# Performance work log

Measured on AMD Instinct MI355X. Metric: run time of the kernel, lower is better.

## Reference

```python
import jax, jax.numpy as jnp
import numpy as np

NUM_SLOTS = 24
EPS = 1e-5

def setup_inputs() -> dict:
    key = jax.random.key(0)
    k1, k2 = jax.random.split(key)
    x = jax.random.normal(k1, (4, 32, 200, 2048), dtype=jnp.float32)
    time = jax.random.randint(k2, (4, 2048), 0, NUM_SLOTS, dtype=jnp.int64)
    return {"x": x, "time": time}

def reference(x, time):
    # x: [b, c, n, t]; time: [b, t] int slot ids in [0, NUM_SLOTS)
    b, c, n, t = x.shape
    time = time[..., -t:]
    idx = time.reshape(b * t)

    # [b*t, n, c] layout matching x.permute(2,0,3,1).reshape(n, b*t, c) contraction
    xf = jnp.transpose(x, (0, 3, 2, 1)).reshape(b * t, n * c)

    # True segment-sum replaces the one-hot matmul; column L1-normalize == divide by slot count
    counts = jax.ops.segment_sum(jnp.ones((b * t,), x.dtype), idx, num_segments=NUM_SLOTS)
    denom = jnp.maximum(counts, 1e-12)[:, None]  # F.normalize eps-clamped norm

    sum_x = jax.ops.segment_sum(xf, idx, num_segments=NUM_SLOTS)            # [S, n*c]
    sum_x2 = jax.ops.segment_sum(xf * xf, idx, num_segments=NUM_SLOTS)      # [S, n*c]

    mean_slot = (sum_x / denom).reshape(NUM_SLOTS, n, c).mean(axis=1)       # [S, c]
    m2_slot = (sum_x2 / denom).reshape(NUM_SLOTS, n, c).mean(axis=1)        # [S, c]
    var_slot = m2_slot - mean_slot ** 2                                     # [S, c]

    # Embedding gather back per (b, t), broadcast over n
    sm = jnp.transpose(mean_slot[time], (0, 2, 1))[:, :, None, :]           # [b, c, 1, t]
    sv = jnp.transpose(var_slot[time], (0, 2, 1))[:, :, None, :]            # [b, c, 1, t]

    return (x - sm) / jnp.sqrt(sv + EPS)
```

## Files before the change

### kernel.cpp

```cpp
#include <hip/hip_runtime.h>
#include <math.h>

#define Bb 4
#define Cc 32
#define Nn 200
#define Tt 2048
#define Ss 24
#define EPSf 1e-5f

typedef float f4 __attribute__((ext_vector_type(4)));
typedef int i4 __attribute__((ext_vector_type(4)));


__global__ __launch_bounds__(1024) void k_prep(const int* __restrict__ timei,
                                               float* __restrict__ gss,
                                               int* __restrict__ hist) {
    __shared__ int lh[Ss];
    const int tid = threadIdx.x;
    if (tid < Ss) lh[tid] = 0;
    for (int i = tid; i < 2 * Ss * Cc; i += 1024) gss[i] = 0.0f;
    __syncthreads();
    for (int i = tid; i < Bb * Tt; i += 1024) atomicAdd(&lh[timei[i]], 1);
    __syncthreads();
    if (tid < Ss) hist[tid] = lh[tid];
}

__global__ __launch_bounds__(256) void k_partial(const float* __restrict__ x,
                                                 const int* __restrict__ timei,
                                                 float* __restrict__ gsum,
                                                 float* __restrict__ gsq) {
    __shared__ float lsum[Ss];
    __shared__ float lsq[Ss];
    const int tid = threadIdx.x;
    const int bx  = blockIdx.x;
    const int tt = bx & 1;
    const int nc = (bx >> 1) & 7;
    const int bc = bx >> 4;
    const int b  = bc >> 5;
    const int c  = bc & 31;

    if (tid < Ss) { lsum[tid] = 0.0f; lsq[tid] = 0.0f; }
    __syncthreads();

    const int t0 = tt * 1024 + tid * 4;
    const i4 sl = *(const i4*)(timei + b * Tt + t0);

    const float* base = x + ((size_t)((b * Cc + c) * Nn)) * Tt + t0;
    float s0 = 0.f, s1 = 0.f, s2 = 0.f, s3 = 0.f;
    float q0 = 0.f, q1 = 0.f, q2 = 0.f, q3 = 0.f;
    const int n0 = nc * 25;
#pragma unroll 5
    for (int n = n0; n < n0 + 25; ++n) {
        f4 v = *(const f4*)(base + (size_t)n * Tt);
        s0 += v[0]; q0 += v[0] * v[0];
        s1 += v[1]; q1 += v[1] * v[1];
        s2 += v[2]; q2 += v[2] * v[2];
        s3 += v[3]; q3 += v[3] * v[3];
    }
    atomicAdd(&lsum[sl[0]], s0); atomicAdd(&lsq[sl[0]], q0);
    atomicAdd(&lsum[sl[1]], s1); atomicAdd(&lsq[sl[1]], q1);
    atomicAdd(&lsum[sl[2]], s2); atomicAdd(&lsq[sl[2]], q2);
    atomicAdd(&lsum[sl[3]], s3); atomicAdd(&lsq[sl[3]], q3);
    __syncthreads();

    if (tid < Ss) {
        atomicAdd(&gsum[tid * Cc + c], lsum[tid]);
        atomicAdd(&gsq[tid * Cc + c], lsq[tid]);
    }
}

__global__ __launch_bounds__(256) void k_norm(const float* __restrict__ x,
                                              const int* __restrict__ timei,
                                              const float* __restrict__ gsum,
                                              const float* __restrict__ gsq,
                                              const int* __restrict__ hist,
                                              float* __restrict__ out) {
    __shared__ float sm[Ss];
    __shared__ float sr[Ss];
    __shared__ float mt[Tt];
    __shared__ float rt[Tt];
    const int tid = threadIdx.x;
    const int idx = (Bb * Cc * 25 - 1) - blockIdx.x;
    const int nchunk = idx % 25;
    const int c = (idx / 25) & 31;
    const int b = idx / (25 * 32);

    if (tid < Ss) {
        float cnt   = (float)hist[tid];
        float denom = fmaxf(cnt, 1e-12f) * (float)Nn;
        float m     = gsum[tid * Cc + c] / denom;
        float m2    = gsq[tid * Cc + c] / denom;
        sm[tid] = m;
        sr[tid] = 1.0f / sqrtf(m2 - m * m + EPSf);
    }
    __syncthreads();

    for (int t = tid; t < Tt; t += 256) {
        const int s = timei[b * Tt + t];
        mt[t] = sm[s];
        rt[t] = sr[s];
    }
    __syncthreads();

    const size_t plane = (size_t)(b * Cc + c) * Nn;
    const int nbeg = nchunk * 8;
#pragma unroll
    for (int n = nbeg; n < nbeg + 8; ++n) {
        const float* xr = x + (plane + n) * Tt;
        float* orow = out + (plane + n) * Tt;
        for (int t4 = tid * 4; t4 < Tt; t4 += 1024) {
            f4 v = *(const f4*)(xr + t4);
            f4 m = *(const f4*)(&mt[t4]);
            f4 r = *(const f4*)(&rt[t4]);
            f4 o;
            o[0] = (v[0] - m[0]) * r[0];
            o[1] = (v[1] - m[1]) * r[1];
            o[2] = (v[2] - m[2]) * r[2];
            o[3] = (v[3] - m[3]) * r[3];
            __builtin_nontemporal_store(o, (f4*)(orow + t4));
        }
    }
}

extern "C" void kernel_launch(void* const* d_in, const int* in_sizes, int n_in,
                              void* d_out, int out_size, void* d_ws, size_t ws_size,
                              hipStream_t stream) {
    const float* x   = (const float*)d_in[0];
    const int* timei = (const int*)d_in[1];
    float* out  = (float*)d_out;
    float* ws   = (float*)d_ws;
    float* gsum = ws;
    float* gsq  = ws + Ss * Cc;
    int*   hist = (int*)(ws + 2 * Ss * Cc);

    k_prep<<<1, 1024, 0, stream>>>(timei, ws, hist);
    k_partial<<<2048, 256, 0, stream>>>(x, timei, gsum, gsq);
    k_norm<<<Bb * Cc * 25, 256, 0, stream>>>(x, timei, gsum, gsq, hist, out);
}
```

Measured before the change: 120.3 us.

## Drop prep kernel, write per-chunk partials, reduce stats inside normalize blocks

Removes the single-block prep kernel by folding the slot histogram into a subset of stats blocks and replacing global float atomics with per-chunk partial writes. The normalize kernel now reduces those partials itself and computes per-slot scale and shift. It also keeps per-thread slot coefficients in registers rather than staging per-t tables in shared memory, and uses an FMA form. Normalize blocks are much larger (50 rows each, 512 blocks), which cuts redundant partial reductions but lowers parallelism and tail flexibility.

```diff
diff --git a/kernel.cpp b/kernel.cpp
--- a/kernel.cpp
+++ b/kernel.cpp
@@ -12,25 +12,12 @@
 typedef int i4 __attribute__((ext_vector_type(4)));
 
 
-__global__ __launch_bounds__(1024) void k_prep(const int* __restrict__ timei,
-                                               float* __restrict__ gss,
-                                               int* __restrict__ hist) {
-    __shared__ int lh[Ss];
-    const int tid = threadIdx.x;
-    if (tid < Ss) lh[tid] = 0;
-    for (int i = tid; i < 2 * Ss * Cc; i += 1024) gss[i] = 0.0f;
-    __syncthreads();
-    for (int i = tid; i < Bb * Tt; i += 1024) atomicAdd(&lh[timei[i]], 1);
-    __syncthreads();
-    if (tid < Ss) hist[tid] = lh[tid];
-}
-
-__global__ __launch_bounds__(256) void k_partial(const float* __restrict__ x,
-                                                 const int* __restrict__ timei,
-                                                 float* __restrict__ gsum,
-                                                 float* __restrict__ gsq) {
-    __shared__ float lsum[Ss];
-    __shared__ float lsq[Ss];
+__global__ __launch_bounds__(256) void k_stats(const float* __restrict__ x,
+                                               const int* __restrict__ timei,
+                                               float2* __restrict__ part,
+                                               int* __restrict__ cntpart) {
+    __shared__ float lsum[Ss], lsq[Ss];
+    __shared__ int   lcnt[Ss];
     const int tid = threadIdx.x;
     const int bx  = blockIdx.x;
     const int tt = bx & 1;
@@ -38,87 +25,114 @@
     const int bc = bx >> 4;
     const int b  = bc >> 5;
     const int c  = bc & 31;
+    const bool do_hist = (c == 0 && nc == 0);
 
-    if (tid < Ss) { lsum[tid] = 0.0f; lsq[tid] = 0.0f; }
+    if (tid < Ss) { lsum[tid] = 0.f; lsq[tid] = 0.f; lcnt[tid] = 0; }
     __syncthreads();
 
     const int t0 = tt * 1024 + tid * 4;
     const i4 sl = *(const i4*)(timei + b * Tt + t0);
 
-    const float* base = x + ((size_t)((b * Cc + c) * Nn)) * Tt + t0;
+    const size_t plane = ((size_t)(b * Cc + c) * Nn + (size_t)nc * 25) * Tt;
+    const float* bp = x + plane + t0;
+
     float s0 = 0.f, s1 = 0.f, s2 = 0.f, s3 = 0.f;
     float q0 = 0.f, q1 = 0.f, q2 = 0.f, q3 = 0.f;
-    const int n0 = nc * 25;
 #pragma unroll 5
-    for (int n = n0; n < n0 + 25; ++n) {
-        f4 v = *(const f4*)(base + (size_t)n * Tt);
+    for (int r = 0; r < 25; ++r) {
+        f4 v = *(const f4*)(bp + (size_t)r * Tt);
         s0 += v[0]; q0 += v[0] * v[0];
         s1 += v[1]; q1 += v[1] * v[1];
         s2 += v[2]; q2 += v[2] * v[2];
         s3 += v[3]; q3 += v[3] * v[3];
     }
+
     atomicAdd(&lsum[sl[0]], s0); atomicAdd(&lsq[sl[0]], q0);
     atomicAdd(&lsum[sl[1]], s1); atomicAdd(&lsq[sl[1]], q1);
     atomicAdd(&lsum[sl[2]], s2); atomicAdd(&lsq[sl[2]], q2);
     atomicAdd(&lsum[sl[3]], s3); atomicAdd(&lsq[sl[3]], q3);
+    if (do_hist) {
+        atomicAdd(&lcnt[sl[0]], 1); atomicAdd(&lcnt[sl[1]], 1);
+        atomicAdd(&lcnt[sl[2]], 1); atomicAdd(&lcnt[sl[3]], 1);
+    }
     __syncthreads();
 
+    const int chunk = (b * 2 + tt) * 8 + nc;
     if (tid < Ss) {
-        atomicAdd(&gsum[tid * Cc + c], lsum[tid]);
-        atomicAdd(&gsq[tid * Cc + c], lsq[tid]);
+        part[(c * Ss + tid) * 64 + chunk] = make_float2(lsum[tid], lsq[tid]);
+        if (do_hist) cntpart[(b * 2 + tt) * Ss + tid] = lcnt[tid];
     }
 }
 
 __global__ __launch_bounds__(256) void k_norm(const float* __restrict__ x,
                                               const int* __restrict__ timei,
-                                              const float* __restrict__ gsum,
-                                              const float* __restrict__ gsq,
-                                              const int* __restrict__ hist,
+                                              const float2* __restrict__ part,
+                                              const int* __restrict__ cntpart,
                                               float* __restrict__ out) {
-    __shared__ float sm[Ss];
-    __shared__ float sr[Ss];
-    __shared__ float mt[Tt];
-    __shared__ float rt[Tt];
+    __shared__ float lsum[Ss], lsq[Ss];
+    __shared__ float s_mr[Ss], s_r[Ss];
     const int tid = threadIdx.x;
-    const int idx = (Bb * Cc * 25 - 1) - blockIdx.x;
-    const int nchunk = idx % 25;
-    const int c = (idx / 25) & 31;
-    const int b = idx / (25 * 32);
+    const int bx  = blockIdx.x;
+    const int b  = bx >> 7;
+    const int c  = (bx >> 2) & 31;
+    const int nc = bx & 3;
 
+    if (tid < Ss) { lsum[tid] = 0.f; lsq[tid] = 0.f; }
+    __syncthreads();
+    if (tid < 192) {
+        const int s = tid >> 3, j = tid & 7;
+        const float2* pp = &part[(c * Ss + s) * 64 + j * 8];
+        float ps = 0.f, pq = 0.f;
+#pragma unroll
+        for (int k = 0; k < 8; ++k) { ps += pp[k].x; pq += pp[k].y; }
+        atomicAdd(&lsum[s], ps);
+        atomicAdd(&lsq[s],  pq);
+    }
+    __syncthreads();
     if (tid < Ss) {
-        float cnt   = (float)hist[tid];
-        float denom = fmaxf(cnt, 1e-12f) * (float)Nn;
-        float m     = gsum[tid * Cc + c] / denom;
-        float m2    = gsq[tid * Cc + c] / denom;
-        sm[tid] = m;
-        sr[tid] = 1.0f / sqrtf(m2 - m * m + EPSf);
+        int cnt = 0;
+#pragma unroll
+        for (int h = 0; h < 8; ++h) cnt += cntpart[h * Ss + tid];
+        float denom = fmaxf((float)cnt, 1e-12f) * (float)Nn;
+        float m  = lsum[tid] / denom;
+        float m2 = lsq[tid]  / denom;
+        float rr = 1.0f / sqrtf(m2 - m * m + EPSf);
+        s_r[tid]  = rr;
+        s_mr[tid] = m * rr;
     }
     __syncthreads();
 
-    for (int t = tid; t < Tt; t += 256) {
-        const int s = timei[b * Tt + t];
-        mt[t] = sm[s];
-        rt[t] = sr[s];
-    }
-    __syncthreads();
+    const int t0 = tid * 4;
+    const i4 sl0 = *(const i4*)(timei + b * Tt + t0);
+    const i4 sl1 = *(const i4*)(timei + b * Tt + t0 + 1024);
+    const float rr0 = s_r[sl0[0]], mr0 = s_mr[sl0[0]];
+    const float rr1 = s_r[sl0[1]], mr1 = s_mr[sl0[1]];
+    const float rr2 = s_r[sl0[2]], mr2 = s_mr[sl0[2]];
+    const float rr3 = s_r[sl0[3]], mr3 = s_mr[sl0[3]];
+    const float rr4 = s_r[sl1[0]], mr4 = s_mr[sl1[0]];
+    const float rr5 = s_r[sl1[1]], mr5 = s_mr[sl1[1]];
+    const float rr6 = s_r[sl1[2]], mr6 = s_mr[sl1[2]];
+    const float rr7 = s_r[sl1[3]], mr7 = s_mr[sl1[3]];
 
-    const size_t plane = (size_t)(b * Cc + c) * Nn;
-    const int nbeg = nchunk * 8;
-#pragma unroll
-    for (int n = nbeg; n < nbeg + 8; ++n) {
-        const float* xr = x + (plane + n) * Tt;
-        float* orow = out + (plane + n) * Tt;
-        for (int t4 = tid * 4; t4 < Tt; t4 += 1024) {
-            f4 v = *(const f4*)(xr + t4);
-            f4 m = *(const f4*)(&mt[t4]);
-            f4 r = *(const f4*)(&rt[t4]);
-            f4 o;
-            o[0] = (v[0] - m[0]) * r[0];
-            o[1] = (v[1] - m[1]) * r[1];
-            o[2] = (v[2] - m[2]) * r[2];
-            o[3] = (v[3] - m[3]) * r[3];
-            __builtin_nontemporal_store(o, (f4*)(orow + t4));
-        }
+    const size_t plane = ((size_t)(b * Cc + c) * Nn + (size_t)nc * 50) * Tt;
+    const float* xp = x + plane + t0;
+    float* op = out + plane + t0;
+
+#pragma unroll 5
+    for (int r = 0; r < 50; ++r) {
+        f4 v0 = *(const f4*)(xp + (size_t)r * Tt);
+        f4 v1 = *(const f4*)(xp + (size_t)r * Tt + 1024);
+        f4 o0, o1;
+        o0[0] = fmaf(v0[0], rr0, -mr0);
+        o0[1] = fmaf(v0[1], rr1, -mr1);
+        o0[2] = fmaf(v0[2], rr2, -mr2);
+        o0[3] = fmaf(v0[3], rr3, -mr3);
+        o1[0] = fmaf(v1[0], rr4, -mr4);
+        o1[1] = fmaf(v1[1], rr5, -mr5);
+        o1[2] = fmaf(v1[2], rr6, -mr6);
+        o1[3] = fmaf(v1[3], rr7, -mr7);
+        __builtin_nontemporal_store(o0, (f4*)(op + (size_t)r * Tt));
+        __builtin_nontemporal_store(o1, (f4*)(op + (size_t)r * Tt + 1024));
     }
 }
 
@@ -127,13 +141,11 @@
                               hipStream_t stream) {
     const float* x   = (const float*)d_in[0];
     const int* timei = (const int*)d_in[1];
-    float* out  = (float*)d_out;
-    float* ws   = (float*)d_ws;
-    float* gsum = ws;
-    float* gsq  = ws + Ss * Cc;
-    int*   hist = (int*)(ws + 2 * Ss * Cc);
+    float* out = (float*)d_out;
 
-    k_prep<<<1, 1024, 0, stream>>>(timei, ws, hist);
-    k_partial<<<2048, 256, 0, stream>>>(x, timei, gsum, gsq);
-    k_norm<<<Bb * Cc * 25, 256, 0, stream>>>(x, timei, gsum, gsq, hist, out);
+    float2* part = (float2*)d_ws;
+    int* cnt = (int*)((char*)d_ws + (size_t)Cc * Ss * 64 * sizeof(float2));
+
+    k_stats<<<2048, 256, 0, stream>>>(x, timei, part, cnt);
+    k_norm<<<512, 256, 0, stream>>>(x, timei, part, cnt, out);
 }
```

Result: faster. 104.2 us (-13.4%).
